# Performance work log

Hardware: AMD Instinct MI355X
Metric: run time of the kernel (lower is better)

The kernel has to match this reference:

```python
import jax, jax.numpy as jnp
import numpy as np

B, L_VLM, L_EXP = 4, 768, 64
L_TOT = L_VLM + L_EXP
D_VLM, D_EXP = 2048, 1024
H, DH = 8, 256
ROPE_BASE = 10000.0
SCALE = 1.0 / np.sqrt(DH).astype(np.float32)


def setup_inputs() -> dict:
    key = jax.random.key(0)
    ks = jax.random.split(key, 12)
    s = 0.02  # weight init scale
    return {
        "vlm_hidden": jax.random.normal(ks[0], (B, L_VLM, D_VLM), jnp.float32),
        "exp_hidden": jax.random.normal(ks[1], (B, L_EXP, D_EXP), jnp.float32),
        "attention_mask": jnp.zeros((B, 1, L_TOT, L_TOT), jnp.float32),  # additive mask
        "position_ids": jnp.broadcast_to(jnp.arange(L_TOT, dtype=jnp.int32)[None, :], (B, L_TOT)),
        "wq_v": jax.random.normal(ks[2], (D_VLM, H * DH), jnp.float32) * s,
        "wk_v": jax.random.normal(ks[3], (D_VLM, H * DH), jnp.float32) * s,
        "wv_v": jax.random.normal(ks[4], (D_VLM, H * DH), jnp.float32) * s,
        "wo_v": jax.random.normal(ks[5], (H * DH, D_VLM), jnp.float32) * s,
        "wq_e": jax.random.normal(ks[6], (D_EXP, H * DH), jnp.float32) * s,
        "wk_e": jax.random.normal(ks[7], (D_EXP, H * DH), jnp.float32) * s,
        "wv_e": jax.random.normal(ks[8], (D_EXP, H * DH), jnp.float32) * s,
        "wo_e": jax.random.normal(ks[9], (H * DH, D_EXP), jnp.float32) * s,
    }


def _proj(hs, w):
    # [B, L, D] @ [D, H*DH] -> [B, H, L, DH]
    b, l, _ = hs.shape
    return jnp.einsum('bld,de->ble', hs, w).reshape(b, l, H, DH).transpose(0, 2, 1, 3)


def _rope(x, cos, sin):
    # NeoX-style rotate-half (Gemma / vLLM RotaryEmbedding with rotary_dim == head_dim)
    d2 = x.shape[-1] // 2
    x1, x2 = x[..., :d2], x[..., d2:]
    return jnp.concatenate([x1 * cos - x2 * sin, x2 * cos + x1 * sin], axis=-1)


def reference(vlm_hidden, exp_hidden, attention_mask, position_ids,
              wq_v, wk_v, wv_v, wo_v, wq_e, wk_e, wv_e, wo_e):
    # 1) separate per-stream Q/K/V projections, 2) concat along sequence dim
    q = jnp.concatenate([_proj(vlm_hidden, wq_v), _proj(exp_hidden, wq_e)], axis=2)
    k = jnp.concatenate([_proj(vlm_hidden, wk_v), _proj(exp_hidden, wk_e)], axis=2)
    v = jnp.concatenate([_proj(vlm_hidden, wv_v), _proj(exp_hidden, wv_e)], axis=2)

    # 3) rotary positional embedding on the joint sequence
    inv_freq = 1.0 / (ROPE_BASE ** (jnp.arange(0, DH, 2, dtype=jnp.float32) / DH))  # [DH/2]
    freqs = position_ids.astype(jnp.float32)[:, :, None] * inv_freq                 # [B, L, DH/2]
    cos = jnp.cos(freqs)[:, None]  # [B, 1, L, DH/2]
    sin = jnp.sin(freqs)[:, None]
    q = _rope(q, cos, sin)
    k = _rope(k, cos, sin)

    # 4) masked attention over the joint sequence
    scores = jnp.einsum('bhqd,bhkd->bhqk', q, k) * SCALE + attention_mask
    probs = jax.nn.softmax(scores, axis=-1)
    out = jnp.einsum('bhqk,bhkd->bhqd', probs, v)              # [B, H, L, DH]
    out = out.transpose(0, 2, 1, 3).reshape(B, L_TOT, H * DH)  # [B, L, H*DH]

    # 5) split back and apply per-stream output projections
    vlm_out = jnp.einsum('ble,ed->bld', out[:, :L_VLM], wo_v)
    exp_out = jnp.einsum('ble,ed->bld', out[:, L_VLM:], wo_e)
    return vlm_out, exp_out
```

## Files before the change

### kernel.cpp

```cpp
#include <hip/hip_runtime.h>

typedef unsigned short u16;
using bf16x8 = __attribute__((ext_vector_type(8))) __bf16;
using f32x4  = __attribute__((ext_vector_type(4))) float;

__device__ __forceinline__ u16 f2bf(float f) {
  unsigned u = __builtin_bit_cast(unsigned, f);
  u += 0x7FFFu + ((u >> 16) & 1u);
  return (u16)(u >> 16);
}
__device__ __forceinline__ float bf2f(u16 s) {
  unsigned u = ((unsigned)s) << 16;
  return __builtin_bit_cast(float, u);
}
__device__ __forceinline__ void lds16(const void* g, void* l) {
  __builtin_amdgcn_global_load_lds(
      (const __attribute__((address_space(1))) void*)g,
      (__attribute__((address_space(3))) void*)l, 16, 0, 0);
}

#define MM(A, B, C) __builtin_amdgcn_mfma_f32_16x16x32_bf16(A, B, C, 0, 0, 0)

#define STG6(TT, QQ) \
  lds16(aS0 + (size_t)(TT) * 32, As + (QQ) * 8192 + t * 8); \
  lds16(aS1 + (size_t)(TT) * 32, As + (QQ) * 8192 + 2048 + t * 8); \
  lds16(aS2 + (size_t)(TT) * 32, As + (QQ) * 8192 + 4096 + t * 8); \
  lds16(aS3 + (size_t)(TT) * 32, As + (QQ) * 8192 + 6144 + t * 8); \
  lds16(bS0 + (size_t)(TT) * 32, Bs + (QQ) * 4096 + t * 8); \
  lds16(bS1 + (size_t)(TT) * 32, Bs + (QQ) * 4096 + 2048 + t * 8);

__device__ __forceinline__ void gemm_w4(
    const u16* aS0, const u16* aS1, const u16* aS2, const u16* aS3,
    const u16* bS0, const u16* bS1,
    int NT, int t, u16* As, u16* Bs, f32x4 (&acc)[8][4])
{
  const int lane = t & 63, fr = lane & 15, q4 = lane >> 4;
  const int w = t >> 6, wm = w >> 1, wn = w & 1;
  const int sxy = (q4 ^ ((fr >> 1) & 3)) * 8;
  const int aoff = (wm * 128 + fr) * 32 + sxy;
  const int boff = (wn * 64 + fr) * 32 + sxy;

  STG6(0, 0);
  STG6(1, 1);
  asm volatile("s_waitcnt vmcnt(6)" ::: "memory");
  __builtin_amdgcn_s_barrier();

  for (int T = 0; T < NT; ++T) {
    const int q = T % 3;
    const u16* Ab = As + q * 8192;
    const u16* Bb = Bs + q * 4096;
    bf16x8 af[8], bfv[4];
#pragma unroll
    for (int mt = 0; mt < 8; ++mt)
      af[mt] = *(const bf16x8*)(Ab + aoff + mt * 512);
#pragma unroll
    for (int nt = 0; nt < 4; ++nt)
      bfv[nt] = *(const bf16x8*)(Bb + boff + nt * 512);
    const bool s2 = (T + 2 < NT);
    if (s2) { const int q2 = (T + 2) % 3; STG6(T + 2, q2); }
    asm volatile("s_waitcnt lgkmcnt(0)" ::: "memory");
    __builtin_amdgcn_sched_barrier(0);
    __builtin_amdgcn_s_setprio(1);
#pragma unroll
    for (int mt = 0; mt < 8; ++mt)
#pragma unroll
      for (int nt = 0; nt < 4; ++nt)
        acc[mt][nt] = MM(af[mt], bfv[nt], acc[mt][nt]);
    __builtin_amdgcn_s_setprio(0);
    if (s2) asm volatile("s_waitcnt vmcnt(6)" ::: "memory");
    else    asm volatile("s_waitcnt vmcnt(0)" ::: "memory");
    __builtin_amdgcn_s_barrier();
  }
}

struct PrepArgs {
  const float* tsrc[8]; u16* tdst[8]; int tK[8]; int tN[8];
  const float* csrc[2]; u16* cdst[2]; int cn4[2];
};

__global__ __launch_bounds__(256) void g_prep(PrepArgs a)
{
  __shared__ float T[32][33];
  const int z = blockIdx.z;
  if (z < 8) {
    const int Krows = a.tK[z], Ncols = a.tN[z];
    const int k0 = blockIdx.y * 32, n0 = blockIdx.x * 32;
    if (k0 >= Krows || n0 >= Ncols) return;
    const float* W = a.tsrc[z];
    u16* Wt = a.tdst[z];
    const int tx = threadIdx.x & 31, ty = threadIdx.x >> 5;
#pragma unroll
    for (int r = 0; r < 4; ++r)
      T[ty + r * 8][tx] = W[(size_t)(k0 + ty + r * 8) * Ncols + n0 + tx];
    __syncthreads();
#pragma unroll
    for (int r = 0; r < 4; ++r)
      Wt[(size_t)(n0 + ty + r * 8) * Krows + k0 + tx] = f2bf(T[tx][ty + r * 8]);
  } else {
    const int j = z - 8;
    const int n4 = a.cn4[j];
    const float* X = a.csrc[j];
    u16* Y = a.cdst[j];
    const int blk = blockIdx.y * gridDim.x + blockIdx.x;
    const int stride = gridDim.x * gridDim.y * 256;
    for (int i = blk * 256 + threadIdx.x; i < n4; i += stride) {
      float4 f = ((const float4*)X)[i];
      ushort4 u;
      u.x = f2bf(f.x); u.y = f2bf(f.y); u.z = f2bf(f.z); u.w = f2bf(f.w);
      ((ushort4*)Y)[i] = u;
    }
  }
}

__global__ __launch_bounds__(256, 2) void g_proj_qkv(
    const u16* __restrict__ Xv, const u16* __restrict__ Xe,
    const u16* __restrict__ Wv_cat, const u16* __restrict__ We_cat,
    u16* __restrict__ Qb, u16* __restrict__ Kb, u16* __restrict__ Vt)
{
  __shared__ __align__(16) u16 As[24576], Bs[12288];
  const int y = blockIdx.y;
  const u16* X; const u16* Wt; int Kdim, rows_pb, l_off, m0;
  if (y < 12) { X = Xv; Wt = Wv_cat; Kdim = 2048; rows_pb = 768; l_off = 0; m0 = y * 256; }
  else        { X = Xe; Wt = We_cat; Kdim = 1024; rows_pb = 64;  l_off = 768; m0 = 0; }
  const int t = threadIdx.x;
  const int n0 = blockIdx.x * 128;
  const int r0 = t >> 2;
  const int swk = ((t & 3) ^ ((t >> 3) & 3)) * 8;
  const u16* aS0 = X + (size_t)(m0 + r0) * Kdim + swk;
  const u16* aS1 = X + (size_t)(m0 + r0 + 64) * Kdim + swk;
  const u16* aS2 = X + (size_t)(m0 + r0 + 128) * Kdim + swk;
  const u16* aS3 = X + (size_t)(m0 + r0 + 192) * Kdim + swk;
  const u16* bS0 = Wt + (size_t)(n0 + r0) * Kdim + swk;
  const u16* bS1 = Wt + (size_t)(n0 + r0 + 64) * Kdim + swk;

  f32x4 acc[8][4] = {};
  gemm_w4(aS0, aS1, aS2, aS3, bS0, bS1, Kdim >> 5, t, As, Bs, acc);

  const int lane = t & 63, fr = lane & 15, q4 = lane >> 4;
  const int w = t >> 6, wm = w >> 1, wn = w & 1;
  const int rbase = m0 + wm * 128 + q4 * 4;
  const int cbase = n0 + wn * 64 + fr;
  const int sect = n0 >> 11;

  if (sect < 2) {
    u16* Out = (sect == 0) ? Qb : Kb;
#pragma unroll
    for (int mt = 0; mt < 8; ++mt) {
#pragma unroll
      for (int rr = 0; rr < 4; ++rr) {
        int m = rbase + mt * 16 + rr;
        int b = m / rows_pb;
        int l = m - b * rows_pb + l_off;
#pragma unroll
        for (int nt = 0; nt < 4; ++nt) {
          int nloc = (cbase + nt * 16) & 2047;
          Out[(((size_t)(b * 8 + (nloc >> 8))) * 832 + l) * 256 + (nloc & 255)] =
              f2bf(acc[mt][nt][rr]);
        }
      }
    }
  } else {
#pragma unroll
    for (int mt = 0; mt < 8; ++mt) {
      int mb = rbase + mt * 16;
      int b = mb / rows_pb;
      int l = mb - b * rows_pb + l_off;
#pragma unroll
      for (int nt = 0; nt < 4; ++nt) {
        int nloc = (cbase + nt * 16) & 2047;
        ushort4 p;
        p.x = f2bf(acc[mt][nt][0]); p.y = f2bf(acc[mt][nt][1]);
        p.z = f2bf(acc[mt][nt][2]); p.w = f2bf(acc[mt][nt][3]);
        *(ushort4*)&Vt[(((size_t)(b * 8 + (nloc >> 8))) * 256 + (nloc & 255)) * 832 + l] = p;
      }
    }
  }
}

__global__ __launch_bounds__(128) void g_rope(
    u16* __restrict__ Q, u16* __restrict__ Kx, const int* __restrict__ pos)
{
  const int blk = blockIdx.x;
  const int l = blk % 832, bh = blk / 832, b = bh >> 3;
  const int i = threadIdx.x;
  const float p = (float)pos[b * 832 + l];
  const float inv = exp2f(-(float)i * 0.103810252965229910f);
  const float ang = p * inv;
  const float c = cosf(ang), s = sinf(ang);
  const size_t base = ((size_t)bh * 832 + l) * 256;

  float x1 = bf2f(Q[base + i]), x2 = bf2f(Q[base + i + 128]);
  Q[base + i]       = f2bf((x1 * c - x2 * s) * 0.0625f);
  Q[base + i + 128] = f2bf((x2 * c + x1 * s) * 0.0625f);
  x1 = bf2f(Kx[base + i]); x2 = bf2f(Kx[base + i + 128]);
  Kx[base + i]       = f2bf(x1 * c - x2 * s);
  Kx[base + i + 128] = f2bf(x2 * c + x1 * s);
}

__global__ __launch_bounds__(256) void g_flash(
    const u16* __restrict__ Qb, const u16* __restrict__ Kb,
    const u16* __restrict__ Vt, const float* __restrict__ mask,
    u16* __restrict__ AO)
{
  __shared__ __align__(16) u16 Ks[2][8192];
  __shared__ __align__(16) u16 Vs[2][8192];
  __shared__ __align__(16) u16 Ps[2048];
  const int t = threadIdx.x;
  const int lane = t & 63, w = t >> 6, quad = lane >> 4;
  const int wb = w * 512;

  const int id = blockIdx.x;
  const int x = id & 7, k = id >> 3;
  const int bh = x + 8 * (k / 13);
  const int q0 = (k % 13) * 64;
  const int b = bh >> 3, h = bh & 7;

  const u16* Ksrc = Kb + (size_t)bh * 832 * 256;
  const u16* Vsrc = Vt + (size_t)bh * 256 * 832;
  const float* Mrow = mask + (size_t)b * 832 * 832;

#define STGK(KT, BUF) \
  _Pragma("unroll") \
  for (int p = 0; p < 4; ++p) { \
    int c = p * 256 + t; \
    int row = c >> 5, chk = c & 31; \
    lds16(Ksrc + (size_t)((KT) * 32 + row) * 256 + ((chk ^ (row & 7)) * 8), \
          Ks[BUF] + c * 8); \
  }
#define STGV(KT, BUF) \
  _Pragma("unroll") \
  for (int p = 0; p < 4; ++p) { \
    int c = p * 256 + t; \
    int row = c >> 3; \
    int lc = (c & 7) ^ (row & 7); \
    int dh = 2 * row + (lc >> 2); \
    lds16(Vsrc + (size_t)dh * 832 + (KT) * 32 + (lc & 3) * 8, Vs[BUF] + c * 8); \
  }

  bf16x8 qf[8];
#pragma unroll
  for (int kf = 0; kf < 8; ++kf)
    qf[kf] = *(const bf16x8*)(
        Qb + ((size_t)bh * 832 + q0 + w * 16 + (lane & 15)) * 256 +
        kf * 32 + quad * 8);

  float lsum[4] = {0.f, 0.f, 0.f, 0.f};
  f32x4 oa[16] = {};

  STGK(0, 0); STGV(0, 0);
  asm volatile("s_waitcnt vmcnt(0)" ::: "memory");
  __builtin_amdgcn_s_barrier();

  for (int kt = 0; kt < 26; ++kt) {
    const int buf = kt & 1;
    if (kt + 1 < 26) { STGK(kt + 1, buf ^ 1); STGV(kt + 1, buf ^ 1); }

    float mv[4][2];
#pragma unroll
    for (int r = 0; r < 4; ++r) {
      int q = q0 + w * 16 + quad * 4 + r;
      const float* mrp = Mrow + (size_t)q * 832 + kt * 32 + (lane & 15);
      mv[r][0] = mrp[0];
      mv[r][1] = mrp[16];
    }

    f32x4 sa[2] = {};
#pragma unroll
    for (int ks = 0; ks < 8; ++ks)
#pragma unroll
      for (int nt = 0; nt < 2; ++nt) {
        int krow = nt * 16 + (lane & 15);
        bf16x8 kb = *(const bf16x8*)(
            Ks[buf] + krow * 256 + (((ks * 4 + quad) ^ (krow & 7)) * 8));
        sa[nt] = MM(qf[ks], kb, sa[nt]);
      }

#pragma unroll
    for (int r = 0; r < 4; ++r) {
      int prow = quad * 4 + r;
      float p0 = __expf(sa[0][r] + mv[r][0]);
      float p1 = __expf(sa[1][r] + mv[r][1]);
      lsum[r] += p0 + p1;
      int s0 = ((lane >> 3) & 1) ^ quad;
      int s1 = (2 | ((lane >> 3) & 1)) ^ quad;
      Ps[wb + prow * 32 + s0 * 8 + (lane & 7)] = f2bf(p0);
      Ps[wb + prow * 32 + s1 * 8 + (lane & 7)] = f2bf(p1);
    }

    int prow2 = lane & 15;
    bf16x8 pa = *(const bf16x8*)(
        Ps + wb + prow2 * 32 + ((quad ^ ((prow2 >> 2) & 3)) * 8));
#pragma unroll
    for (int nt = 0; nt < 16; ++nt) {
      int dh = nt * 16 + (lane & 15);
      int row = dh >> 1;
      int lc = ((dh & 1) << 2) | quad;
      bf16x8 vb = *(const bf16x8*)(Vs[buf] + row * 64 + ((lc ^ (row & 7)) * 8));
      oa[nt] = MM(pa, vb, oa[nt]);
    }

    asm volatile("s_waitcnt vmcnt(0)" ::: "memory");
    __builtin_amdgcn_s_barrier();
  }

  float linv[4];
#pragma unroll
  for (int r = 0; r < 4; ++r) {
    float s = lsum[r];
    s += __shfl_xor(s, 1);
    s += __shfl_xor(s, 2);
    s += __shfl_xor(s, 4);
    s += __shfl_xor(s, 8);
    linv[r] = 1.0f / s;
  }
#pragma unroll
  for (int r = 0; r < 4; ++r) {
    size_t l = q0 + w * 16 + quad * 4 + r;
    u16* dst = AO + ((size_t)b * 832 + l) * 2048 + h * 256 + (lane & 15);
#pragma unroll
    for (int nt = 0; nt < 16; ++nt)
      dst[nt * 16] = f2bf(oa[nt][r] * linv[r]);
  }
#undef STGK
#undef STGV
}

__global__ __launch_bounds__(256, 2) void g_oproj2(
    const u16* __restrict__ AO, const u16* __restrict__ Wov,
    const u16* __restrict__ Woe, float* __restrict__ out)
{
  __shared__ __align__(16) u16 As[24576], Bs[12288];
  const int y = blockIdx.y;
  const u16* Wt; float* C; int N, rows_pb, l_off, m0;
  if (y < 12) { Wt = Wov; C = out; N = 2048; rows_pb = 768; l_off = 0; m0 = y * 256; }
  else {
    if (blockIdx.x >= 8) return;
    Wt = Woe; C = out + (size_t)4 * 768 * 2048; N = 1024; rows_pb = 64; l_off = 768; m0 = 0;
  }
  const int t = threadIdx.x;
  const int n0 = blockIdx.x * 128;
  const int r0 = t >> 2;
  const int swk = ((t & 3) ^ ((t >> 3) & 3)) * 8;
  const u16* aSp[4];
#pragma unroll
  for (int i = 0; i < 4; ++i) {
    int mr = m0 + i * 64 + r0;
    int ba = mr / rows_pb;
    aSp[i] = AO + ((size_t)ba * 832 + (mr - ba * rows_pb) + l_off) * 2048 + swk;
  }
  const u16* bS0 = Wt + (size_t)(n0 + r0) * 2048 + swk;
  const u16* bS1 = Wt + (size_t)(n0 + r0 + 64) * 2048 + swk;

  f32x4 acc[8][4] = {};
  gemm_w4(aSp[0], aSp[1], aSp[2], aSp[3], bS0, bS1, 64, t, As, Bs, acc);

  const int lane = t & 63, fr = lane & 15, q4 = lane >> 4;
  const int w = t >> 6, wm = w >> 1, wn = w & 1;
  const int rbase = m0 + wm * 128 + q4 * 4;
  const int cbase = n0 + wn * 64 + fr;
#pragma unroll
  for (int mt = 0; mt < 8; ++mt)
#pragma unroll
    for (int rr = 0; rr < 4; ++rr) {
      size_t m = rbase + mt * 16 + rr;
#pragma unroll
      for (int nt = 0; nt < 4; ++nt)
        C[m * N + cbase + nt * 16] = acc[mt][nt][rr];
    }
}

extern "C" void kernel_launch(void* const* d_in, const int* in_sizes, int n_in,
                              void* d_out, int out_size, void* d_ws, size_t ws_size,
                              hipStream_t stream)
{
  const float* vlm_h = (const float*)d_in[0];
  const float* exp_h = (const float*)d_in[1];
  const float* mask  = (const float*)d_in[2];
  const int*   pos   = (const int*)d_in[3];
  const float* wq_v  = (const float*)d_in[4];
  const float* wk_v  = (const float*)d_in[5];
  const float* wv_v  = (const float*)d_in[6];
  const float* wo_v  = (const float*)d_in[7];
  const float* wq_e  = (const float*)d_in[8];
  const float* wk_e  = (const float*)d_in[9];
  const float* wv_e  = (const float*)d_in[10];
  const float* wo_e  = (const float*)d_in[11];
  float* out = (float*)d_out;

  u16* U = (u16*)d_ws;
  u16* Xv   = U; U += (size_t)4 * 768 * 2048;
  u16* Xe   = U; U += (size_t)4 * 64 * 1024;
  u16* Wcv  = U; U += (size_t)6144 * 2048;
  u16* Wce  = U; U += (size_t)6144 * 1024;
  u16* Wov  = U; U += (size_t)2048 * 2048;
  u16* Woe  = U; U += (size_t)1024 * 2048;
  u16* Qb   = U; U += (size_t)32 * 832 * 256;
  u16* Kb   = U; U += (size_t)32 * 832 * 256;
  u16* Vt   = U; U += (size_t)32 * 256 * 832;
  u16* AO   = U; U += (size_t)4 * 832 * 2048;

  const dim3 blk(256);

  PrepArgs pa;
  pa.tsrc[0] = wq_v; pa.tdst[0] = Wcv;                        pa.tK[0] = 2048; pa.tN[0] = 2048;
  pa.tsrc[1] = wk_v; pa.tdst[1] = Wcv + (size_t)2048 * 2048;  pa.tK[1] = 2048; pa.tN[1] = 2048;
  pa.tsrc[2] = wv_v; pa.tdst[2] = Wcv + (size_t)4096 * 2048;  pa.tK[2] = 2048; pa.tN[2] = 2048;
  pa.tsrc[3] = wo_v; pa.tdst[3] = Wov;                        pa.tK[3] = 2048; pa.tN[3] = 2048;
  pa.tsrc[4] = wq_e; pa.tdst[4] = Wce;                        pa.tK[4] = 1024; pa.tN[4] = 2048;
  pa.tsrc[5] = wk_e; pa.tdst[5] = Wce + (size_t)2048 * 1024;  pa.tK[5] = 1024; pa.tN[5] = 2048;
  pa.tsrc[6] = wv_e; pa.tdst[6] = Wce + (size_t)4096 * 1024;  pa.tK[6] = 1024; pa.tN[6] = 2048;
  pa.tsrc[7] = wo_e; pa.tdst[7] = Woe;                        pa.tK[7] = 2048; pa.tN[7] = 1024;
  pa.csrc[0] = vlm_h; pa.cdst[0] = Xv; pa.cn4[0] = 1572864;
  pa.csrc[1] = exp_h; pa.cdst[1] = Xe; pa.cn4[1] = 65536;
  g_prep<<<dim3(64, 64, 10), blk, 0, stream>>>(pa);

  g_proj_qkv<<<dim3(48, 13, 1), blk, 0, stream>>>(Xv, Xe, Wcv, Wce, Qb, Kb, Vt);

  g_rope<<<dim3(32 * 832), dim3(128), 0, stream>>>(Qb, Kb, pos);

  g_flash<<<dim3(416), blk, 0, stream>>>(Qb, Kb, Vt, mask, AO);

  g_oproj2<<<dim3(16, 13, 1), blk, 0, stream>>>(AO, Wov, Woe, out);
}
```

Before: 393.3 us.

## Use 256x256 tiles with 8-wave ping-pong schedule in QKV projection

Replaces the QKV projection GEMM with a 512-thread block computing a 256x256 output tile, using double-buffered LDS and a four-phase loop that interleaves global-to-LDS loads with MFMA groups. It raises s_setprio around the MFMA groups. The larger tile increases operand reuse and halves the grid in the N direction, aiming to cut global/LDS traffic and hide load latency. In exchange it adds many more barriers per K step, and launch_bounds(512,4) with 64 KB of LDS per block may limit occupancy.

```diff
diff --git a/kernel.cpp b/kernel.cpp
--- a/kernel.cpp
+++ b/kernel.cpp
@@ -20,6 +20,85 @@
 }
 
 #define MM(A, B, C) __builtin_amdgcn_mfma_f32_16x16x32_bf16(A, B, C, 0, 0, 0)
+
+#define PH_TOP() \
+  __builtin_amdgcn_s_barrier(); \
+  asm volatile("s_waitcnt lgkmcnt(0)" ::: "memory"); \
+  __builtin_amdgcn_sched_barrier(0);
+
+#define MFMA8(MA, MB) \
+  __builtin_amdgcn_s_setprio(1); \
+  acc[MA][0] = MM(a0, b0, acc[MA][0]); \
+  acc[MA][1] = MM(a0, b1, acc[MA][1]); \
+  acc[MA][2] = MM(a0, b2, acc[MA][2]); \
+  acc[MA][3] = MM(a0, b3, acc[MA][3]); \
+  acc[MB][0] = MM(a1, b0, acc[MB][0]); \
+  acc[MB][1] = MM(a1, b1, acc[MB][1]); \
+  acc[MB][2] = MM(a1, b2, acc[MB][2]); \
+  acc[MB][3] = MM(a1, b3, acc[MB][3]); \
+  __builtin_amdgcn_s_setprio(0);
+
+__device__ __forceinline__ void gemm2(
+    const u16* aS0, const u16* aS1, const u16* bS0, const u16* bS1,
+    int NT, int t, u16* As, u16* Bs, f32x4 (&acc)[8][4])
+{
+  const int lane = t & 63, fr = lane & 15, q4 = lane >> 4;
+  const int w = t >> 6, wm = w >> 2, wn = w & 3;
+  const int sxy = (q4 ^ ((fr >> 1) & 3)) * 8;
+  const int aoff = (wm * 128 + fr) * 32 + sxy;
+  const int boff = (wn * 64 + fr) * 32 + sxy;
+
+  lds16(aS0, As + t * 8);
+  lds16(aS1, As + 4096 + t * 8);
+  lds16(bS0, Bs + t * 8);
+  lds16(bS1, Bs + 4096 + t * 8);
+  asm volatile("s_waitcnt vmcnt(0)" ::: "memory");
+  __builtin_amdgcn_s_barrier();
+
+  for (int T = 0; T < NT; ++T) {
+    const int pb = T & 1;
+    const u16* Ab = As + pb * 8192;
+    const u16* Bb = Bs + pb * 8192;
+    u16* An = As + (pb ^ 1) * 8192;
+    u16* Bn = Bs + (pb ^ 1) * 8192;
+    const bool s1 = (T + 1 < NT);
+    const size_t k1 = (size_t)(T + 1) * 32;
+    bf16x8 a0, a1, b0, b1, b2, b3;
+
+    a0 = *(const bf16x8*)(Ab + aoff);
+    a1 = *(const bf16x8*)(Ab + aoff + 512);
+    b0 = *(const bf16x8*)(Bb + boff);
+    b1 = *(const bf16x8*)(Bb + boff + 512);
+    b2 = *(const bf16x8*)(Bb + boff + 1024);
+    b3 = *(const bf16x8*)(Bb + boff + 1536);
+    if (s1) lds16(aS0 + k1, An + t * 8);
+    PH_TOP();
+    MFMA8(0, 1);
+    __builtin_amdgcn_s_barrier();
+
+    a0 = *(const bf16x8*)(Ab + aoff + 1024);
+    a1 = *(const bf16x8*)(Ab + aoff + 1536);
+    if (s1) lds16(aS1 + k1, An + 4096 + t * 8);
+    PH_TOP();
+    MFMA8(2, 3);
+    __builtin_amdgcn_s_barrier();
+
+    a0 = *(const bf16x8*)(Ab + aoff + 2048);
+    a1 = *(const bf16x8*)(Ab + aoff + 2560);
+    if (s1) lds16(bS0 + k1, Bn + t * 8);
+    PH_TOP();
+    MFMA8(4, 5);
+    __builtin_amdgcn_s_barrier();
+
+    a0 = *(const bf16x8*)(Ab + aoff + 3072);
+    a1 = *(const bf16x8*)(Ab + aoff + 3584);
+    if (s1) lds16(bS1 + k1, Bn + 4096 + t * 8);
+    PH_TOP();
+    MFMA8(6, 7);
+    if (s1) asm volatile("s_waitcnt vmcnt(0)" ::: "memory");
+    __builtin_amdgcn_s_barrier();
+  }
+}
 
 #define STG6(TT, QQ) \
   lds16(aS0 + (size_t)(TT) * 32, As + (QQ) * 8192 + t * 8); \
@@ -112,34 +191,32 @@
   }
 }
 
-__global__ __launch_bounds__(256, 2) void g_proj_qkv(
+__global__ __launch_bounds__(512, 4) void g_proj_qkv(
     const u16* __restrict__ Xv, const u16* __restrict__ Xe,
     const u16* __restrict__ Wv_cat, const u16* __restrict__ We_cat,
     u16* __restrict__ Qb, u16* __restrict__ Kb, u16* __restrict__ Vt)
 {
-  __shared__ __align__(16) u16 As[24576], Bs[12288];
+  __shared__ __align__(16) u16 As[16384], Bs[16384];
   const int y = blockIdx.y;
   const u16* X; const u16* Wt; int Kdim, rows_pb, l_off, m0;
   if (y < 12) { X = Xv; Wt = Wv_cat; Kdim = 2048; rows_pb = 768; l_off = 0; m0 = y * 256; }
   else        { X = Xe; Wt = We_cat; Kdim = 1024; rows_pb = 64;  l_off = 768; m0 = 0; }
   const int t = threadIdx.x;
-  const int n0 = blockIdx.x * 128;
+  const int n0 = blockIdx.x * 256;
   const int r0 = t >> 2;
-  const int swk = ((t & 3) ^ ((t >> 3) & 3)) * 8;
+  const int swk = ((t & 3) ^ ((r0 >> 1) & 3)) * 8;
   const u16* aS0 = X + (size_t)(m0 + r0) * Kdim + swk;
-  const u16* aS1 = X + (size_t)(m0 + r0 + 64) * Kdim + swk;
-  const u16* aS2 = X + (size_t)(m0 + r0 + 128) * Kdim + swk;
-  const u16* aS3 = X + (size_t)(m0 + r0 + 192) * Kdim + swk;
+  const u16* aS1 = X + (size_t)(m0 + r0 + 128) * Kdim + swk;
   const u16* bS0 = Wt + (size_t)(n0 + r0) * Kdim + swk;
-  const u16* bS1 = Wt + (size_t)(n0 + r0 + 64) * Kdim + swk;
+  const u16* bS1 = Wt + (size_t)(n0 + r0 + 128) * Kdim + swk;
 
   f32x4 acc[8][4] = {};
-  gemm_w4(aS0, aS1, aS2, aS3, bS0, bS1, Kdim >> 5, t, As, Bs, acc);
-
-  const int lane = t & 63, fr = lane & 15, q4 = lane >> 4;
-  const int w = t >> 6, wm = w >> 1, wn = w & 1;
+  gemm2(aS0, aS1, bS0, bS1, Kdim >> 5, t, As, Bs, acc);
+
+  const int lane = t & 63, q4 = lane >> 4;
+  const int wn = (t >> 6) & 3, wm = t >> 8;
   const int rbase = m0 + wm * 128 + q4 * 4;
-  const int cbase = n0 + wn * 64 + fr;
+  const int cbase = n0 + wn * 64 + (lane & 15);
   const int sect = n0 >> 11;
 
   if (sect < 2) {
@@ -147,15 +224,15 @@
 #pragma unroll
     for (int mt = 0; mt < 8; ++mt) {
 #pragma unroll
-      for (int rr = 0; rr < 4; ++rr) {
-        int m = rbase + mt * 16 + rr;
+      for (int r = 0; r < 4; ++r) {
+        int m = rbase + mt * 16 + r;
         int b = m / rows_pb;
         int l = m - b * rows_pb + l_off;
 #pragma unroll
         for (int nt = 0; nt < 4; ++nt) {
           int nloc = (cbase + nt * 16) & 2047;
           Out[(((size_t)(b * 8 + (nloc >> 8))) * 832 + l) * 256 + (nloc & 255)] =
-              f2bf(acc[mt][nt][rr]);
+              f2bf(acc[mt][nt][r]);
         }
       }
     }
@@ -414,7 +491,7 @@
   pa.csrc[1] = exp_h; pa.cdst[1] = Xe; pa.cn4[1] = 65536;
   g_prep<<<dim3(64, 64, 10), blk, 0, stream>>>(pa);
 
-  g_proj_qkv<<<dim3(48, 13, 1), blk, 0, stream>>>(Xv, Xe, Wcv, Wce, Qb, Kb, Vt);
+  g_proj_qkv<<<dim3(24, 13, 1), dim3(512), 0, stream>>>(Xv, Xe, Wcv, Wce, Qb, Kb, Vt);
 
   g_rope<<<dim3(32 * 832), dim3(128), 0, stream>>>(Qb, Kb, pos);
 
```

New measurement: 1.041 ms. 165% more time.
